# Optimization experiments

Hardware: AMD Instinct MI355X
Metric: run time of the kernel (lower is better)

## Reference

```python
import jax, jax.numpy as jnp
import numpy as np

WS = 7      # window size
SS = 3      # shift size
NH = 6      # num heads
C = 192     # dim
B = 32
HH = 112
WW = 112


def _rel_pos_index(ws):
    coords = np.stack(np.meshgrid(np.arange(ws), np.arange(ws), indexing='ij'))
    cf = coords.reshape(2, -1)
    rel = (cf[:, :, None] - cf[:, None, :]).transpose(1, 2, 0)
    rel[:, :, 0] += ws - 1
    rel[:, :, 1] += ws - 1
    rel[:, :, 0] *= 2 * ws - 1
    return rel.sum(-1)  # (N, N) int


def _attn_mask(H, W, ws, ss):
    # standard Swin SW-MSA mask: -100 where tokens come from different regions
    img = np.zeros((H, W))
    cnt = 0
    for h in (slice(0, -ws), slice(-ws, -ss), slice(-ss, None)):
        for w in (slice(0, -ws), slice(-ws, -ss), slice(-ss, None)):
            img[h, w] = cnt
            cnt += 1
    mw = img.reshape(H // ws, ws, W // ws, ws).transpose(0, 2, 1, 3).reshape(-1, ws * ws)
    diff = mw[:, None, :] - mw[:, :, None]
    return np.where(diff != 0, -100.0, 0.0).astype(np.float32)  # (nW, N, N)


def _ln(x, g, b, eps=1e-5):
    m = x.mean(-1, keepdims=True)
    v = ((x - m) ** 2).mean(-1, keepdims=True)
    return (x - m) * jax.lax.rsqrt(v + eps) * g + b


def setup_inputs() -> dict:
    key = jax.random.key(0)
    ks = jax.random.split(key, 8)
    hid = 4 * C
    nbias = (2 * WS - 1) * (2 * WS - 1)
    return {
        'x': jax.random.normal(ks[0], (B, HH * WW, C), dtype=jnp.float32),
        'norm1_g': jnp.ones((C,), jnp.float32),
        'norm1_b': jnp.zeros((C,), jnp.float32),
        'qkv_w': jax.random.normal(ks[1], (3 * C, C), jnp.float32) * 0.02,
        'qkv_b': jnp.zeros((3 * C,), jnp.float32),
        'rpb_table': jax.random.normal(ks[2], (nbias, NH), jnp.float32) * 0.02,
        'proj_w': jax.random.normal(ks[3], (C, C), jnp.float32) * 0.02,
        'proj_b': jnp.zeros((C,), jnp.float32),
        'norm2_g': jnp.ones((C,), jnp.float32),
        'norm2_b': jnp.zeros((C,), jnp.float32),
        'fc1_w': jax.random.normal(ks[4], (hid, C), jnp.float32) * 0.02,
        'fc1_b': jnp.zeros((hid,), jnp.float32),
        'fc2_w': jax.random.normal(ks[5], (C, hid), jnp.float32) * 0.02,
        'fc2_b': jnp.zeros((C,), jnp.float32),
        'H': HH,
        'W': WW,
    }


def reference(x, norm1_g, norm1_b, qkv_w, qkv_b, rpb_table, proj_w, proj_b,
              norm2_g, norm2_b, fc1_w, fc1_b, fc2_w, fc2_b, H, W):
    Bb, L, Cc = x.shape
    N = WS * WS
    hd = Cc // NH
    rpi = jnp.asarray(_rel_pos_index(WS))                      # (N, N)
    amask = jnp.asarray(_attn_mask(H, W, WS, SS))              # (nW, N, N)
    nW = amask.shape[0]

    shortcut = x
    h = _ln(x, norm1_g, norm1_b).reshape(Bb, H, W, Cc)
    # cyclic shift
    h = jnp.roll(h, shift=(-SS, -SS), axis=(1, 2))
    # window partition -> (B*nW, N, C)
    h = h.reshape(Bb, H // WS, WS, W // WS, WS, Cc).transpose(0, 1, 3, 2, 4, 5)
    xw = h.reshape(-1, N, Cc)
    Bn = xw.shape[0]

    qkv = (xw @ qkv_w.T + qkv_b).reshape(Bn, N, 3, NH, hd).transpose(2, 0, 3, 1, 4)
    q, k, v = qkv[0], qkv[1], qkv[2]                           # (Bn, NH, N, hd)
    q = q * (hd ** -0.5)
    attn = jnp.einsum('bhnd,bhmd->bhnm', q, k)                 # (Bn, NH, N, N)
    bias = rpb_table[rpi.reshape(-1)].reshape(N, N, NH).transpose(2, 0, 1)
    attn = attn + bias[None]
    attn = (attn.reshape(Bb, nW, NH, N, N) + amask[None, :, None]).reshape(Bn, NH, N, N)
    attn = jax.nn.softmax(attn, axis=-1)
    out = jnp.einsum('bhnm,bhmd->bhnd', attn, v).transpose(0, 2, 1, 3).reshape(Bn, N, Cc)
    out = out @ proj_w.T + proj_b

    # window reverse + reverse cyclic shift
    out = out.reshape(Bb, H // WS, W // WS, WS, WS, Cc).transpose(0, 1, 3, 2, 4, 5).reshape(Bb, H, W, Cc)
    out = jnp.roll(out, shift=(SS, SS), axis=(1, 2)).reshape(Bb, L, Cc)

    x = shortcut + out
    y = _ln(x, norm2_g, norm2_b)
    y = jax.nn.gelu(y @ fc1_w.T + fc1_b, approximate=False) @ fc2_w.T + fc2_b
    return x + y
```

## Files before the change

kernel.cpp:

```cpp
#include <hip/hip_runtime.h>
#include <stdint.h>
#include <math.h>


typedef unsigned short u16;
typedef unsigned int   u32;
typedef __bf16 v8bf __attribute__((ext_vector_type(8)));
typedef float  v4f  __attribute__((ext_vector_type(4)));
typedef u16    v8u16 __attribute__((ext_vector_type(8)));
typedef u16    v4u16 __attribute__((ext_vector_type(4)));

#define MFMA16(a,b,c) __builtin_amdgcn_mfma_f32_16x16x32_bf16(a,b,c,0,0,0)

#define HSTR 77070336L
#define QSC  0.17677669529663687f

__device__ __forceinline__ u16 f2bf(float f){
  return __builtin_bit_cast(u16, (__bf16)f);
}

__device__ __forceinline__ void async16(void* lds, const void* g){
  __builtin_amdgcn_global_load_lds(
      (__attribute__((address_space(1))) void*)(g),
      (__attribute__((address_space(3))) void*)(lds), 16, 0, 0);
}

__global__ __launch_bounds__(256)
void convw(const float* __restrict__ s0, const float* __restrict__ s1,
           const float* __restrict__ s2, const float* __restrict__ s3,
           u16* __restrict__ d){
  int i = blockIdx.x * 256 + threadIdx.x;
  float v;
  if (i < 110592){
    v = s0[i];
    if (i < 36864) v *= QSC;
  }
  else if (i < 147456)  v = s1[i - 110592];
  else if (i < 294912)  v = s2[i - 147456];
  else                  v = s3[i - 294912];
  d[i] = f2bf(v);
}

__global__ __launch_bounds__(256)
void bmt_k(const float* __restrict__ rpb, float* __restrict__ bmt){
  int idx = blockIdx.x * 256 + threadIdx.x;
  int r  = idx & 3, lg = (idx >> 2) & 3, lr = (idx >> 4) & 15;
  int n  = (idx >> 8) & 3, m = (idx >> 10) & 3;
  int t  = idx >> 12; int h = t % 6, cls = t / 6;
  int row = m*16 + lg*4 + r, col = n*16 + lr;
  float v;
  if (row >= 49 || col >= 49){
    v = -1e30f;
  } else {
    int i1 = row / 7, j1 = row - i1 * 7;
    int i2 = col / 7, j2 = col - i2 * 7;
    int ridx = (i1 - i2 + 6) * 13 + (j1 - j2 + 6);
    v = rpb[ridx * 6 + h];
    int lh1 = (cls & 2) ? (i1 < 4 ? 1 : 2) : 0;
    int lw1 = (cls & 1) ? (j1 < 4 ? 1 : 2) : 0;
    int lh2 = (cls & 2) ? (i2 < 4 ? 1 : 2) : 0;
    int lw2 = (cls & 1) ? (j2 < 4 ? 1 : 2) : 0;
    if (lh1 * 3 + lw1 != lh2 * 3 + lw2) v -= 100.f;
  }
  bmt[idx] = v;
}

template<bool GATHER>
__global__ __launch_bounds__(256)
void ln_kern(const float* __restrict__ x, const float* __restrict__ g,
             const float* __restrict__ b, u16* __restrict__ o){
  const int ts  = threadIdx.x >> 4;
  const int l16 = threadIdx.x & 15;
  const int r   = blockIdx.x * 16 + ts;
  const float* src;
  if (GATHER){
    u32 wdx = (u32)r / 49u; int nn = r - (int)wdx * 49;
    int bb = (int)(wdx >> 8); int wl = (int)(wdx & 255);
    int wh = wl >> 4, wwi = wl & 15;
    int ii = (int)((u32)nn / 7u), jj = nn - ii * 7;
    int th = wh * 7 + ii + 3;  if (th >= 112) th -= 112;
    int tw = wwi * 7 + jj + 3; if (tw >= 112) tw -= 112;
    src = x + (u32)(bb * 12544 + th * 112 + tw) * 192u;
  } else {
    src = x + (u32)r * 192u;
  }
  const float4 a0 = *(const float4*)(src + l16*12);
  const float4 a1 = *(const float4*)(src + l16*12 + 4);
  const float4 a2 = *(const float4*)(src + l16*12 + 8);
  float sm = ((a0.x+a0.y)+(a0.z+a0.w)) + ((a1.x+a1.y)+(a1.z+a1.w))
           + ((a2.x+a2.y)+(a2.z+a2.w));
  float sq = ((a0.x*a0.x+a0.y*a0.y)+(a0.z*a0.z+a0.w*a0.w))
           + ((a1.x*a1.x+a1.y*a1.y)+(a1.z*a1.z+a1.w*a1.w))
           + ((a2.x*a2.x+a2.y*a2.y)+(a2.z*a2.z+a2.w*a2.w));
  #pragma unroll
  for (int d = 1; d < 16; d <<= 1){
    sm += __shfl_xor(sm, d, 64);
    sq += __shfl_xor(sq, d, 64);
  }
  float mean = sm * (1.f/192.f);
  float var  = sq * (1.f/192.f) - mean * mean;
  float rs   = rsqrtf(var + 1e-5f);
  const float4 g0 = *(const float4*)(g + l16*12);
  const float4 g1 = *(const float4*)(g + l16*12 + 4);
  const float4 g2 = *(const float4*)(g + l16*12 + 8);
  const float4 b0 = *(const float4*)(b + l16*12);
  const float4 b1 = *(const float4*)(b + l16*12 + 4);
  const float4 b2 = *(const float4*)(b + l16*12 + 8);
  u16* dst = o + (u32)r * 192u + l16 * 12;
  v4u16 w0, w1, w2;
  w0[0]=f2bf((a0.x-mean)*rs*g0.x+b0.x); w0[1]=f2bf((a0.y-mean)*rs*g0.y+b0.y);
  w0[2]=f2bf((a0.z-mean)*rs*g0.z+b0.z); w0[3]=f2bf((a0.w-mean)*rs*g0.w+b0.w);
  w1[0]=f2bf((a1.x-mean)*rs*g1.x+b1.x); w1[1]=f2bf((a1.y-mean)*rs*g1.y+b1.y);
  w1[2]=f2bf((a1.z-mean)*rs*g1.z+b1.z); w1[3]=f2bf((a1.w-mean)*rs*g1.w+b1.w);
  w2[0]=f2bf((a2.x-mean)*rs*g2.x+b2.x); w2[1]=f2bf((a2.y-mean)*rs*g2.y+b2.y);
  w2[2]=f2bf((a2.z-mean)*rs*g2.z+b2.z); w2[3]=f2bf((a2.w-mean)*rs*g2.w+b2.w);
  *(v4u16*)(dst)     = w0;
  *(v4u16*)(dst + 4) = w1;
  *(v4u16*)(dst + 8) = w2;
}

template<int EPI, int LDA, int LDW>
__global__ __launch_bounds__(512)
void gemm_bt(const u16* __restrict__ A, int aRowOff,
             const u16* __restrict__ W, int K, int ncol,
             const float* __restrict__ bias,
             u16* __restrict__ ob, float* __restrict__ of,
             const float* __restrict__ xres, int oRowOff){
  __shared__ __align__(16) u16 sA[128 * 200];
  __shared__ __align__(16) u16 sW[64 * 200];
  const int tid = threadIdx.x;
  const int wv = tid >> 6, lnn = tid & 63;
  const int lr = lnn & 15, lg = lnn >> 4;
  const int win = 56 * ncol;
  const int grp = (int)blockIdx.x / win, loc = (int)blockIdx.x - grp * win;
  const int rloc = loc % 56, cblk = loc / 56;
  const int m0   = (grp * 56 + rloc) * 128;
  const int col0 = cblk * 64;
  const int wr = wv >> 1, wc = wv & 1;

  const int chb0 = col0 + wc*32 + lg*4;
  const int chb1 = chb0 + 16;
  float4 bv0 = *(const float4*)&bias[chb0];
  float4 bv1 = *(const float4*)&bias[chb1];
  if (EPI == 0){
    if (chb0 < 192){ bv0.x*=QSC; bv0.y*=QSC; bv0.z*=QSC; bv0.w*=QSC; }
    if (chb1 < 192){ bv1.x*=QSC; bv1.y*=QSC; bv1.z*=QSC; bv1.w*=QSC; }
  }
  v4f acc[2][2];
  acc[0][0] = acc[0][1] = (v4f){bv0.x, bv0.y, bv0.z, bv0.w};
  acc[1][0] = acc[1][1] = (v4f){bv1.x, bv1.y, bv1.z, bv1.w};

  const int rA0 = (int)((u32)tid / 25u);
  const int cA0 = tid - rA0 * 25;
  const u32 aBase = (u32)(aRowOff + m0);
  const int nK = K / 192;
  for (int ks = 0; ks < nK; ++ks){
    if (ks) __syncthreads();
    const int k0 = ks * 192;
    int ra = rA0, ca = cA0;
    #pragma unroll
    for (int it = 0; it < 6; ++it){
      int cc = (ca == 24) ? 23 : ca;
      async16((char*)sA + (size_t)(it * 512 + wv * 64) * 16,
              A + (aBase + (u32)ra) * (u32)LDA + (u32)(k0 + cc * 8));
      ra += 20; ca += 12; if (ca >= 25){ ca -= 25; ra += 1; }
    }
    if (tid < 128){
      int cc = (ca == 24) ? 23 : ca;
      async16((char*)sA + (size_t)(3072 + wv * 64) * 16,
              A + (aBase + (u32)ra) * (u32)LDA + (u32)(k0 + cc * 8));
    }
    int rw = rA0, cw = cA0;
    #pragma unroll
    for (int it = 0; it < 3; ++it){
      int cc = (cw == 24) ? 23 : cw;
      async16((char*)sW + (size_t)(it * 512 + wv * 64) * 16,
              W + (u32)(col0 + rw) * (u32)LDW + (u32)(k0 + cc * 8));
      rw += 20; cw += 12; if (cw >= 25){ cw -= 25; rw += 1; }
    }
    if (tid < 64){
      int cc = (cw == 24) ? 23 : cw;
      async16((char*)sW + (size_t)1536 * 16,
              W + (u32)(col0 + rw) * (u32)LDW + (u32)(k0 + cc * 8));
    }
    __syncthreads();

    #pragma unroll
    for (int kk = 0; kk < 6; ++kk){
      v8bf af[2], wf[2];
      #pragma unroll
      for (int m = 0; m < 2; ++m)
        af[m] = *(const v8bf*)&sA[(wr*32 + m*16 + lr) * 200 + kk*32 + lg*8];
      #pragma unroll
      for (int n = 0; n < 2; ++n)
        wf[n] = *(const v8bf*)&sW[(wc*32 + n*16 + lr) * 200 + kk*32 + lg*8];
      #pragma unroll
      for (int n = 0; n < 2; ++n)
        #pragma unroll
        for (int m = 0; m < 2; ++m)
          acc[n][m] = MFMA16(wf[n], af[m], acc[n][m]);
    }
  }

  if (EPI == 0){
    u32 chpart[2];
    const int chbs[2] = {chb0, chb1};
    #pragma unroll
    for (int n = 0; n < 2; ++n){
      int ch = chbs[n];
      int which = (ch >= 384) ? 2 : ((ch >= 192) ? 1 : 0);
      int rem = ch - which * 192;
      chpart[n] = (u32)which * 77070336u + (u32)((rem >> 5) * 1568 + (rem & 31));
    }
    #pragma unroll
    for (int m = 0; m < 2; ++m){
      const int t = m0 + wr*32 + m*16 + lr;
      u32 wdx = (u32)t / 49u; u32 tnn = (u32)t - wdx * 49u;
      const u32 rowpart = wdx * 9408u + tnn * 32u;
      #pragma unroll
      for (int n = 0; n < 2; ++n){
        v4u16 pk;
        pk[0] = f2bf(acc[n][m][0]); pk[1] = f2bf(acc[n][m][1]);
        pk[2] = f2bf(acc[n][m][2]); pk[3] = f2bf(acc[n][m][3]);
        *(v4u16*)&ob[chpart[n] + rowpart] = pk;
      }
    }
  } else if (EPI == 1){
    #pragma unroll
    for (int m = 0; m < 2; ++m){
      const int gr = m0 + wr*32 + m*16 + lr;
      u32 wdx = (u32)gr / 49u; int nn = gr - (int)wdx * 49;
      int bb = (int)(wdx >> 8); int wl = (int)(wdx & 255);
      int wh = wl >> 4, wwi = wl & 15;
      int ii = (int)((u32)nn / 7u), jj = nn - ii * 7;
      int th = wh * 7 + ii + 3;  if (th >= 112) th -= 112;
      int tw = wwi * 7 + jj + 3; if (tw >= 112) tw -= 112;
      u32 adr = (u32)(bb * 12544 + th * 112 + tw) * 192u;
      #pragma unroll
      for (int n = 0; n < 2; ++n){
        u32 a2 = adr + (u32)(n ? chb1 : chb0);
        float4 xv = *(const float4*)&xres[a2];
        float4 ov = {xv.x + acc[n][m][0], xv.y + acc[n][m][1],
                     xv.z + acc[n][m][2], xv.w + acc[n][m][3]};
        *(float4*)&of[a2] = ov;
      }
    }
  } else if (EPI == 3){
    #pragma unroll
    for (int m = 0; m < 2; ++m){
      const u32 base = (u32)(oRowOff + m0 + wr*32 + m*16 + lr) * 192u;
      #pragma unroll
      for (int n = 0; n < 2; ++n){
        u32 a2 = base + (u32)(n ? chb1 : chb0);
        float4 xv = *(const float4*)&of[a2];
        float4 ov = {xv.x + acc[n][m][0], xv.y + acc[n][m][1],
                     xv.z + acc[n][m][2], xv.w + acc[n][m][3]};
        *(float4*)&of[a2] = ov;
      }
    }
  } else {
    #pragma unroll
    for (int m = 0; m < 2; ++m){
      const u32 base = (u32)(m0 + wr*32 + m*16 + lr) * 768u;
      #pragma unroll
      for (int n = 0; n < 2; ++n){
        v4u16 pk;
        #pragma unroll
        for (int r = 0; r < 4; ++r){
          float v = acc[n][m][r];
          pk[r] = f2bf(0.5f * v * (1.0f + erff(v * 0.7071067811865475f)));
        }
        *(v4u16*)&ob[base + (u32)(n ? chb1 : chb0)] = pk;
      }
    }
  }
}

__global__ __launch_bounds__(256, 4)
void attn_k(const u16* __restrict__ qkv, const float* __restrict__ bmt,
            u16* __restrict__ aout){
  __shared__ __align__(16) u16 plds[4][64 * 64];
  const int wv = threadIdx.x >> 6, lnn = threadIdx.x & 63;
  const int lr = lnn & 15, lg = lnn >> 4;
  const u32 gid = (u32)blockIdx.x * 4u + (u32)wv;
  const u32 w = gid / 6u; const int h = (int)(gid - w * 6u);
  const u16* qb = qkv + (size_t)gid * 1568;
  const u16* kb = qb + HSTR;
  const u16* vb = kb + HSTR;

  const int wl = (int)(w & 255);
  const int cls = (((wl >> 4) == 15) ? 2 : 0) | (((wl & 15) == 15) ? 1 : 0);
  const float* bmv = bmt + ((u32)(cls * 6 + h) << 12);
  v4f s[4][4];
  #pragma unroll
  for (int m = 0; m < 4; ++m)
    #pragma unroll
    for (int n = 0; n < 4; ++n)
      s[m][n] = *(const v4f*)&bmv[(u32)(((m*4 + n)*16 + lr)*16 + lg*4)];

  v8bf aq[4], bk4[4];
  #pragma unroll
  for (int m = 0; m < 4; ++m) aq[m]  = *(const v8bf*)(qb + (m*16 + lr)*32 + lg*8);
  #pragma unroll
  for (int n = 0; n < 4; ++n) bk4[n] = *(const v8bf*)(kb + (n*16 + lr)*32 + lg*8);
  #pragma unroll
  for (int m = 0; m < 4; ++m)
    #pragma unroll
    for (int n = 0; n < 4; ++n) s[m][n] = MFMA16(aq[m], bk4[n], s[m][n]);

  v8u16 bvu[2][2];
  #pragma unroll
  for (int n2 = 0; n2 < 2; ++n2)
    #pragma unroll
    for (int ksi = 0; ksi < 2; ++ksi)
      #pragma unroll
      for (int e = 0; e < 8; ++e){
        int kp = ksi * 32 + lg * 8 + e;
        int t  = (kp >> 2) + (kp & 3) * 16;
        bvu[n2][ksi][e] = vb[(u32)(t * 32 + n2 * 16 + lr)];
      }

  #pragma unroll
  for (int m = 0; m < 4; ++m)
    #pragma unroll
    for (int r = 0; r < 4; ++r){
      int row = m*16 + lg*4 + r;
      v4u16 pk;
      pk[0] = f2bf(__expf(s[m][0][r]));
      pk[1] = f2bf(__expf(s[m][1][r]));
      pk[2] = f2bf(__expf(s[m][2][r]));
      pk[3] = f2bf(__expf(s[m][3][r]));
      *(v4u16*)((char*)&plds[wv][0] + row*128 + ((lr*8) ^ ((row & 7) << 4))) = pk;
    }

  v8bf pa[4][2];
  #pragma unroll
  for (int m2 = 0; m2 < 4; ++m2)
    #pragma unroll
    for (int ksi = 0; ksi < 2; ++ksi){
      int row2 = m2*16 + lr;
      pa[m2][ksi] = *(const v8bf*)((const char*)&plds[wv][0] + row2*128 +
                                   ((ksi*64 + lg*16) ^ ((row2 & 7) << 4)));
    }

  v8u16 onesu;
  #pragma unroll
  for (int e = 0; e < 8; ++e) onesu[e] = (u16)0x3F80;
  const v8bf onesf = __builtin_bit_cast(v8bf, onesu);

  const v4f zf = {0.f, 0.f, 0.f, 0.f};
  v4f o2[4][2], sacc[4];
  #pragma unroll
  for (int m2 = 0; m2 < 4; ++m2){
    o2[m2][0] = zf; o2[m2][1] = zf; sacc[m2] = zf;
  }
  #pragma unroll
  for (int ksi = 0; ksi < 2; ++ksi)
    #pragma unroll
    for (int m2 = 0; m2 < 4; ++m2){
      o2[m2][0] = MFMA16(__builtin_bit_cast(v8bf, bvu[0][ksi]), pa[m2][ksi], o2[m2][0]);
      o2[m2][1] = MFMA16(__builtin_bit_cast(v8bf, bvu[1][ksi]), pa[m2][ksi], o2[m2][1]);
      sacc[m2]  = MFMA16(onesf, pa[m2][ksi], sacc[m2]);
    }

  float invl[4];
  #pragma unroll
  for (int m2 = 0; m2 < 4; ++m2) invl[m2] = 1.0f / sacc[m2][0];

  #pragma unroll
  for (int m2 = 0; m2 < 4; ++m2){
    const int token = m2*16 + lr;
    if (token < 49){
      const u32 base = (w * 49u + (u32)token) * 192u + (u32)(h*32 + lg*4);
      #pragma unroll
      for (int n2 = 0; n2 < 2; ++n2){
        v4u16 pk;
        pk[0] = f2bf(o2[m2][n2][0] * invl[m2]);
        pk[1] = f2bf(o2[m2][n2][1] * invl[m2]);
        pk[2] = f2bf(o2[m2][n2][2] * invl[m2]);
        pk[3] = f2bf(o2[m2][n2][3] * invl[m2]);
        *(v4u16*)&aout[base + (u32)(n2*16)] = pk;
      }
    }
  }
}

extern "C" void kernel_launch(void* const* d_in, const int* in_sizes, int n_in,
                              void* d_out, int out_size, void* d_ws, size_t ws_size,
                              hipStream_t stream){
  const float* x     = (const float*)d_in[0];
  const float* n1g   = (const float*)d_in[1];
  const float* n1b   = (const float*)d_in[2];
  const float* qkvw  = (const float*)d_in[3];
  const float* qkvb  = (const float*)d_in[4];
  const float* rpb   = (const float*)d_in[5];
  const float* projw = (const float*)d_in[6];
  const float* projb = (const float*)d_in[7];
  const float* n2g   = (const float*)d_in[8];
  const float* n2b   = (const float*)d_in[9];
  const float* fc1w  = (const float*)d_in[10];
  const float* fc1b  = (const float*)d_in[11];
  const float* fc2w  = (const float*)d_in[12];
  const float* fc2b  = (const float*)d_in[13];
  float* out = (float*)d_out;

  char* ws  = (char*)d_ws;
  u16* bufA = (u16*)ws;
  u16* bufB = (u16*)(ws + 462422016L);
  u16* wq   = (u16*)(ws + 616562688L);
  u16* wp   = wq + 110592;
  u16* w1   = wp + 36864;
  u16* w2   = w1 + 147456;
  float* bmt = (float*)d_out;

  convw<<<1728, 256, 0, stream>>>(qkvw, projw, fc1w, fc2w, wq);
  bmt_k<<<384, 256, 0, stream>>>(rpb, bmt);

  ln_kern<true><<<25088, 256, 0, stream>>>(x, n1g, n1b, bufB);
  gemm_bt<0, 192, 192><<<3136*9, 512, 0, stream>>>(bufB, 0, wq, 192, 9,
                                                   qkvb, bufA, nullptr, nullptr, 0);
  attn_k<<<12288, 256, 0, stream>>>(bufA, bmt, bufB);
  gemm_bt<1, 192, 192><<<3136*3, 512, 0, stream>>>(bufB, 0, wp, 192, 3,
                                                   projb, nullptr, out, x, 0);
  ln_kern<false><<<25088, 256, 0, stream>>>(out, n2g, n2b, bufB);
  for (int c = 0; c < 2; ++c){
    int off = c * 200704;
    gemm_bt<2, 192, 192><<<1568*12, 512, 0, stream>>>(bufB, off, w1, 192, 12,
                                                      fc1b, bufA, nullptr, nullptr, 0);
    gemm_bt<3, 768, 768><<<1568*3, 512, 0, stream>>>(bufA, 0, w2, 768, 3,
                                                     fc2b, nullptr, out, nullptr, off);
  }
}
```

Measured before the change: 1.431 ms.

## Fuse LayerNorm into GEMM prologues and restructure attention output normalization

Measured after the change: 2.286 ms. 59.8% more time.

```diff
diff --git a/kernel.cpp b/kernel.cpp
--- a/kernel.cpp
+++ b/kernel.cpp
@@ -65,67 +65,15 @@
   bmt[idx] = v;
 }
 
-template<bool GATHER>
-__global__ __launch_bounds__(256)
-void ln_kern(const float* __restrict__ x, const float* __restrict__ g,
-             const float* __restrict__ b, u16* __restrict__ o){
-  const int ts  = threadIdx.x >> 4;
-  const int l16 = threadIdx.x & 15;
-  const int r   = blockIdx.x * 16 + ts;
-  const float* src;
-  if (GATHER){
-    u32 wdx = (u32)r / 49u; int nn = r - (int)wdx * 49;
-    int bb = (int)(wdx >> 8); int wl = (int)(wdx & 255);
-    int wh = wl >> 4, wwi = wl & 15;
-    int ii = (int)((u32)nn / 7u), jj = nn - ii * 7;
-    int th = wh * 7 + ii + 3;  if (th >= 112) th -= 112;
-    int tw = wwi * 7 + jj + 3; if (tw >= 112) tw -= 112;
-    src = x + (u32)(bb * 12544 + th * 112 + tw) * 192u;
-  } else {
-    src = x + (u32)r * 192u;
-  }
-  const float4 a0 = *(const float4*)(src + l16*12);
-  const float4 a1 = *(const float4*)(src + l16*12 + 4);
-  const float4 a2 = *(const float4*)(src + l16*12 + 8);
-  float sm = ((a0.x+a0.y)+(a0.z+a0.w)) + ((a1.x+a1.y)+(a1.z+a1.w))
-           + ((a2.x+a2.y)+(a2.z+a2.w));
-  float sq = ((a0.x*a0.x+a0.y*a0.y)+(a0.z*a0.z+a0.w*a0.w))
-           + ((a1.x*a1.x+a1.y*a1.y)+(a1.z*a1.z+a1.w*a1.w))
-           + ((a2.x*a2.x+a2.y*a2.y)+(a2.z*a2.z+a2.w*a2.w));
-  #pragma unroll
-  for (int d = 1; d < 16; d <<= 1){
-    sm += __shfl_xor(sm, d, 64);
-    sq += __shfl_xor(sq, d, 64);
-  }
-  float mean = sm * (1.f/192.f);
-  float var  = sq * (1.f/192.f) - mean * mean;
-  float rs   = rsqrtf(var + 1e-5f);
-  const float4 g0 = *(const float4*)(g + l16*12);
-  const float4 g1 = *(const float4*)(g + l16*12 + 4);
-  const float4 g2 = *(const float4*)(g + l16*12 + 8);
-  const float4 b0 = *(const float4*)(b + l16*12);
-  const float4 b1 = *(const float4*)(b + l16*12 + 4);
-  const float4 b2 = *(const float4*)(b + l16*12 + 8);
-  u16* dst = o + (u32)r * 192u + l16 * 12;
-  v4u16 w0, w1, w2;
-  w0[0]=f2bf((a0.x-mean)*rs*g0.x+b0.x); w0[1]=f2bf((a0.y-mean)*rs*g0.y+b0.y);
-  w0[2]=f2bf((a0.z-mean)*rs*g0.z+b0.z); w0[3]=f2bf((a0.w-mean)*rs*g0.w+b0.w);
-  w1[0]=f2bf((a1.x-mean)*rs*g1.x+b1.x); w1[1]=f2bf((a1.y-mean)*rs*g1.y+b1.y);
-  w1[2]=f2bf((a1.z-mean)*rs*g1.z+b1.z); w1[3]=f2bf((a1.w-mean)*rs*g1.w+b1.w);
-  w2[0]=f2bf((a2.x-mean)*rs*g2.x+b2.x); w2[1]=f2bf((a2.y-mean)*rs*g2.y+b2.y);
-  w2[2]=f2bf((a2.z-mean)*rs*g2.z+b2.z); w2[3]=f2bf((a2.w-mean)*rs*g2.w+b2.w);
-  *(v4u16*)(dst)     = w0;
-  *(v4u16*)(dst + 4) = w1;
-  *(v4u16*)(dst + 8) = w2;
-}
-
 template<int EPI, int LDA, int LDW>
 __global__ __launch_bounds__(512)
 void gemm_bt(const u16* __restrict__ A, int aRowOff,
              const u16* __restrict__ W, int K, int ncol,
              const float* __restrict__ bias,
              u16* __restrict__ ob, float* __restrict__ of,
-             const float* __restrict__ xres, int oRowOff){
+             const float* __restrict__ xres,
+             const float* __restrict__ lng, const float* __restrict__ lnb,
+             int oRowOff){
   __shared__ __align__(16) u16 sA[128 * 200];
   __shared__ __align__(16) u16 sW[64 * 200];
   const int tid = threadIdx.x;
@@ -153,22 +101,72 @@
   const int rA0 = (int)((u32)tid / 25u);
   const int cA0 = tid - rA0 * 25;
   const u32 aBase = (u32)(aRowOff + m0);
+
+  if (EPI == 0 || EPI == 2){
+    const int row = tid >> 2;
+    const int q   = tid & 3;
+    const int gr  = aRowOff + m0 + row;
+    const float* srcp;
+    if (EPI == 0){
+      u32 wdx = (u32)gr / 49u; int nn = gr - (int)wdx * 49;
+      int bb = (int)(wdx >> 8); int wl2 = (int)(wdx & 255);
+      int wh = wl2 >> 4, wwi = wl2 & 15;
+      int ii = (int)((u32)nn / 7u), jj = nn - ii * 7;
+      int th = wh * 7 + ii + 3;  if (th >= 112) th -= 112;
+      int tw = wwi * 7 + jj + 3; if (tw >= 112) tw -= 112;
+      srcp = xres + (u32)(bb * 12544 + th * 112 + tw) * 192u + q * 48;
+    } else {
+      srcp = xres + (u32)gr * 192u + q * 48;
+    }
+    float4 a[12];
+    #pragma unroll
+    for (int i = 0; i < 12; ++i) a[i] = *(const float4*)(srcp + i*4);
+    float sm = 0.f, sq = 0.f;
+    #pragma unroll
+    for (int i = 0; i < 12; ++i){
+      sm += (a[i].x + a[i].y) + (a[i].z + a[i].w);
+      sq += (a[i].x*a[i].x + a[i].y*a[i].y) + (a[i].z*a[i].z + a[i].w*a[i].w);
+    }
+    sm += __shfl_xor(sm, 1, 64);  sq += __shfl_xor(sq, 1, 64);
+    sm += __shfl_xor(sm, 2, 64);  sq += __shfl_xor(sq, 2, 64);
+    float mean = sm * (1.f/192.f);
+    float var  = sq * (1.f/192.f) - mean * mean;
+    float rs   = rsqrtf(var + 1e-5f);
+    #pragma unroll
+    for (int c2 = 0; c2 < 6; ++c2){
+      v8u16 pk;
+      #pragma unroll
+      for (int i = 0; i < 2; ++i){
+        const float4 gv = *(const float4*)(lng + q*48 + c2*8 + i*4);
+        const float4 bv = *(const float4*)(lnb + q*48 + c2*8 + i*4);
+        const float4 av = a[c2*2 + i];
+        pk[i*4+0] = f2bf((av.x - mean) * rs * gv.x + bv.x);
+        pk[i*4+1] = f2bf((av.y - mean) * rs * gv.y + bv.y);
+        pk[i*4+2] = f2bf((av.z - mean) * rs * gv.z + bv.z);
+        pk[i*4+3] = f2bf((av.w - mean) * rs * gv.w + bv.w);
+      }
+      *(v8u16*)&sA[row*200 + q*48 + c2*8] = pk;
+    }
+  }
+
   const int nK = K / 192;
   for (int ks = 0; ks < nK; ++ks){
     if (ks) __syncthreads();
     const int k0 = ks * 192;
-    int ra = rA0, ca = cA0;
-    #pragma unroll
-    for (int it = 0; it < 6; ++it){
-      int cc = (ca == 24) ? 23 : ca;
-      async16((char*)sA + (size_t)(it * 512 + wv * 64) * 16,
-              A + (aBase + (u32)ra) * (u32)LDA + (u32)(k0 + cc * 8));
-      ra += 20; ca += 12; if (ca >= 25){ ca -= 25; ra += 1; }
-    }
-    if (tid < 128){
-      int cc = (ca == 24) ? 23 : ca;
-      async16((char*)sA + (size_t)(3072 + wv * 64) * 16,
-              A + (aBase + (u32)ra) * (u32)LDA + (u32)(k0 + cc * 8));
+    if (EPI == 1 || EPI == 3){
+      int ra = rA0, ca = cA0;
+      #pragma unroll
+      for (int it = 0; it < 6; ++it){
+        int cc = (ca == 24) ? 23 : ca;
+        async16((char*)sA + (size_t)(it * 512 + wv * 64) * 16,
+                A + (aBase + (u32)ra) * (u32)LDA + (u32)(k0 + cc * 8));
+        ra += 20; ca += 12; if (ca >= 25){ ca -= 25; ra += 1; }
+      }
+      if (tid < 128){
+        int cc = (ca == 24) ? 23 : ca;
+        async16((char*)sA + (size_t)(3072 + wv * 64) * 16,
+                A + (aBase + (u32)ra) * (u32)LDA + (u32)(k0 + cc * 8));
+      }
     }
     int rw = rA0, cw = cA0;
     #pragma unroll
@@ -230,8 +228,8 @@
     for (int m = 0; m < 2; ++m){
       const int gr = m0 + wr*32 + m*16 + lr;
       u32 wdx = (u32)gr / 49u; int nn = gr - (int)wdx * 49;
-      int bb = (int)(wdx >> 8); int wl = (int)(wdx & 255);
-      int wh = wl >> 4, wwi = wl & 15;
+      int bb = (int)(wdx >> 8); int wl2 = (int)(wdx & 255);
+      int wh = wl2 >> 4, wwi = wl2 & 15;
       int ii = (int)((u32)nn / 7u), jj = nn - ii * 7;
       int th = wh * 7 + ii + 3;  if (th >= 112) th -= 112;
       int tw = wwi * 7 + jj + 3; if (tw >= 112) tw -= 112;
@@ -345,7 +343,7 @@
 
   v8u16 onesu;
   #pragma unroll
-  for (int e = 0; e < 8; ++e) onesu[e] = (u16)0x3F80;
+  for (int e = 0; e < 8; ++e) onesu[e] = (lr == 0) ? (u16)0x3F80 : (u16)0;
   const v8bf onesf = __builtin_bit_cast(v8bf, onesu);
 
   const v4f zf = {0.f, 0.f, 0.f, 0.f};
@@ -358,28 +356,29 @@
   for (int ksi = 0; ksi < 2; ++ksi)
     #pragma unroll
     for (int m2 = 0; m2 < 4; ++m2){
-      o2[m2][0] = MFMA16(__builtin_bit_cast(v8bf, bvu[0][ksi]), pa[m2][ksi], o2[m2][0]);
-      o2[m2][1] = MFMA16(__builtin_bit_cast(v8bf, bvu[1][ksi]), pa[m2][ksi], o2[m2][1]);
-      sacc[m2]  = MFMA16(onesf, pa[m2][ksi], sacc[m2]);
-    }
-
-  float invl[4];
-  #pragma unroll
-  for (int m2 = 0; m2 < 4; ++m2) invl[m2] = 1.0f / sacc[m2][0];
+      o2[m2][0] = MFMA16(pa[m2][ksi], __builtin_bit_cast(v8bf, bvu[0][ksi]), o2[m2][0]);
+      o2[m2][1] = MFMA16(pa[m2][ksi], __builtin_bit_cast(v8bf, bvu[1][ksi]), o2[m2][1]);
+      sacc[m2]  = MFMA16(pa[m2][ksi], onesf, sacc[m2]);
+    }
+
+  float inv[4][4];
+  #pragma unroll
+  for (int m2 = 0; m2 < 4; ++m2)
+    #pragma unroll
+    for (int r = 0; r < 4; ++r)
+      inv[m2][r] = 1.0f / __shfl(sacc[m2][r], lnn & 48, 64);
 
   #pragma unroll
   for (int m2 = 0; m2 < 4; ++m2){
-    const int token = m2*16 + lr;
-    if (token < 49){
-      const u32 base = (w * 49u + (u32)token) * 192u + (u32)(h*32 + lg*4);
-      #pragma unroll
-      for (int n2 = 0; n2 < 2; ++n2){
-        v4u16 pk;
-        pk[0] = f2bf(o2[m2][n2][0] * invl[m2]);
-        pk[1] = f2bf(o2[m2][n2][1] * invl[m2]);
-        pk[2] = f2bf(o2[m2][n2][2] * invl[m2]);
-        pk[3] = f2bf(o2[m2][n2][3] * invl[m2]);
-        *(v4u16*)&aout[base + (u32)(n2*16)] = pk;
+    #pragma unroll
+    for (int n2 = 0; n2 < 2; ++n2){
+      #pragma unroll
+      for (int r = 0; r < 4; ++r){
+        int row = m2*16 + lg*4 + r;
+        if (row < 49){
+          float val = o2[m2][n2][r] * inv[m2][r];
+          aout[(w * 49u + (u32)row) * 192u + (u32)(h*32 + n2*16 + lr)] = f2bf(val);
+        }
       }
     }
   }
@@ -416,18 +415,20 @@
   convw<<<1728, 256, 0, stream>>>(qkvw, projw, fc1w, fc2w, wq);
   bmt_k<<<384, 256, 0, stream>>>(rpb, bmt);
 
-  ln_kern<true><<<25088, 256, 0, stream>>>(x, n1g, n1b, bufB);
-  gemm_bt<0, 192, 192><<<3136*9, 512, 0, stream>>>(bufB, 0, wq, 192, 9,
-                                                   qkvb, bufA, nullptr, nullptr, 0);
+  gemm_bt<0, 192, 192><<<3136*9, 512, 0, stream>>>(nullptr, 0, wq, 192, 9,
+                                                   qkvb, bufA, nullptr,
+                                                   x, n1g, n1b, 0);
   attn_k<<<12288, 256, 0, stream>>>(bufA, bmt, bufB);
   gemm_bt<1, 192, 192><<<3136*3, 512, 0, stream>>>(bufB, 0, wp, 192, 3,
-                                                   projb, nullptr, out, x, 0);
-  ln_kern<false><<<25088, 256, 0, stream>>>(out, n2g, n2b, bufB);
+                                                   projb, nullptr, out,
+                                                   x, nullptr, nullptr, 0);
   for (int c = 0; c < 2; ++c){
     int off = c * 200704;
-    gemm_bt<2, 192, 192><<<1568*12, 512, 0, stream>>>(bufB, off, w1, 192, 12,
-                                                      fc1b, bufA, nullptr, nullptr, 0);
+    gemm_bt<2, 192, 192><<<1568*12, 512, 0, stream>>>(nullptr, off, w1, 192, 12,
+                                                      fc1b, bufA, nullptr,
+                                                      out, n2g, n2b, 0);
     gemm_bt<3, 768, 768><<<1568*3, 512, 0, stream>>>(bufA, 0, w2, 768, 3,
-                                                     fc2b, nullptr, out, nullptr, off);
-  }
-}
+                                                     fc2b, nullptr, out,
+                                                     nullptr, nullptr, nullptr, off);
+  }
+}
```
